# Performance work log

Hardware: AMD Instinct MI355X
Metric: run time of the kernel (lower is better)

The kernel has to match this reference:

```python
import jax, jax.numpy as jnp
import numpy as np

TEMPERATURE = 1.0
W_BLEND = 0.8
EPS = 1e-12  # torch F.normalize eps


def _l2norm(x):
    n = jnp.sqrt(jnp.sum(x * x, axis=-1, keepdims=True))
    return x / jnp.maximum(n, EPS)


def setup_inputs() -> dict:
    key = jax.random.key(0)
    feats = jax.random.normal(key, (4, 2048, 256), dtype=jnp.float32)
    return {"feats": feats}


def reference(feats):
    B, N, C = feats.shape
    f = _l2norm(feats.reshape(B * N, C))                 # [BN, C], unit rows
    scores = jnp.matmul(f, f.T) / TEMPERATURE            # [BN, BN] cosine sims
    attn = jax.nn.softmax(scores, axis=-1)               # [BN, BN]
    feats_att = jnp.matmul(attn, f)                      # [BN, C]
    feats_fcm = f * W_BLEND + feats_att * (1.0 - W_BLEND)
    return _l2norm(feats_fcm.reshape(B, N, C))           # [B, N, C]
```

## Files before the change

kernel.cpp:

```cpp
#include <hip/hip_runtime.h>

typedef unsigned char u8;
typedef unsigned short u16;
typedef unsigned int u32;
typedef unsigned long long u64;
typedef long long i64;
typedef __attribute__((ext_vector_type(16))) float floatx16;

#define BN 8192
#define DIM 256
#define NSPLIT 8
#define KPS (BN / NSPLIT)
#define BKN 32
#define NIT (KPS / BKN)

__device__ __forceinline__ u16 f2bf(float x) {
    u32 u = __builtin_bit_cast(u32, x);
    u = (u + 0x7fffu + ((u >> 16) & 1u)) >> 16;
    return (u16)u;
}
__device__ __forceinline__ float bf2f(u16 h) {
    return __builtin_bit_cast(float, (u32)h << 16);
}
__device__ __forceinline__ u64 pack4bf(float a, float b, float c, float d) {
    return (u64)f2bf(a) | ((u64)f2bf(b) << 16) | ((u64)f2bf(c) << 32) | ((u64)f2bf(d) << 48);
}
__device__ __forceinline__ u32 pk_fp8(float a, float b, float c, float d) {
    int v = __builtin_amdgcn_cvt_pk_fp8_f32(a, b, 0, false);
    v = __builtin_amdgcn_cvt_pk_fp8_f32(c, d, v, true);
    return (u32)v;
}
__device__ __forceinline__ void gl_lds16(const void* g, void* l) {
    __builtin_amdgcn_global_load_lds(
        (const __attribute__((address_space(1))) u32*)g,
        (__attribute__((address_space(3))) u32*)l, 16, 0, 0);
}
#define MFMA8(A, B, C) __builtin_amdgcn_mfma_f32_32x32x16_fp8_fp8((A), (B), (C), 0, 0, 0)

__global__ __launch_bounds__(256) void k_prep(const float* __restrict__ in,
                                              u8* __restrict__ fb, u8* __restrict__ fv) {
    __shared__ u16 t[32 * 260];
    const int tid = threadIdx.x;
    const int wave = tid >> 6, lane = tid & 63;
    const int kb = blockIdx.x, r0 = kb * 32;
    #pragma unroll
    for (int i = 0; i < 8; ++i) {
        const int rl = wave * 8 + i;
        const float4 v = *(const float4*)(in + (size_t)(r0 + rl) * DIM + lane * 4);
        float ss = v.x * v.x + v.y * v.y + v.z * v.z + v.w * v.w;
        #pragma unroll
        for (int off = 1; off < 64; off <<= 1) ss += __shfl_xor(ss, off, 64);
        const float inv = 1.0f / fmaxf(sqrtf(ss), 1e-12f);
        const float n0 = v.x * inv, n1 = v.y * inv, n2 = v.z * inv, n3 = v.w * inv;
        *(u32*)(fb + (size_t)(r0 + rl) * DIM + lane * 4) = pk_fp8(n0, n1, n2, n3);
        *(u64*)(&t[rl * 260 + lane * 4]) = pack4bf(n0, n1, n2, n3);
    }
    __syncthreads();
    #pragma unroll
    for (int i = 0; i < 4; ++i) {
        const int S = i * 256 + tid;
        const int d = S >> 2;
        const int c = ((S & 3) - (d >> 2)) & 3;
        float f[8];
        #pragma unroll
        for (int j = 0; j < 8; ++j) f[j] = bf2f(t[(8 * c + j) * 260 + d]);
        const u32 lo = pk_fp8(f[0], f[1], f[2], f[3]);
        const u32 hi = pk_fp8(f[4], f[5], f[6], f[7]);
        *(u64*)(fv + (size_t)kb * 8192 + S * 8) = ((u64)hi << 32) | lo;
    }
}

__global__ __launch_bounds__(256, 2) void k_flash(
        const u8* __restrict__ fb, const u8* __restrict__ fv,
        u16* __restrict__ Opart, float* __restrict__ lpart) {
    __shared__ u8 tileK[2][8192];
    __shared__ u8 tileV[2][8192];

    const int tid = threadIdx.x;
    const int wave = tid >> 6, lane = tid & 63;
    const int c31 = lane & 31, g1 = lane >> 5;
    const int split = blockIdx.x & (NSPLIT - 1);
    const int qblk = blockIdx.x >> 3;
    const int q0 = qblk * 128 + wave * 32;
    const int key0 = split * KPS;

    i64 qf[16];
    #pragma unroll
    for (int kc = 0; kc < 16; ++kc)
        qf[kc] = *(const i64*)(fb + (size_t)(q0 + c31) * DIM + kc * 16 + g1 * 8);

    floatx16 o[8];
    #pragma unroll
    for (int i = 0; i < 8; ++i)
        #pragma unroll
        for (int r = 0; r < 16; ++r) o[i][r] = 0.f;
    float lsum = 0.f;

    int offK[2];
    #pragma unroll
    for (int i = 0; i < 2; ++i) {
        const int S = wave * 128 + i * 64 + lane;
        const int r = S >> 4, s = S & 15;
        const int c = (s & 8) | ((s ^ r) & 7);
        offK[i] = r * 256 + c * 16;
    }
    const u8* gK = fb + (size_t)key0 * DIM;
    const u8* gV = fv + (size_t)(key0 >> 5) * 8192;

    auto stage = [&](int s, int b) {
        const size_t oo = (size_t)s * 8192;
        u8* lK = &tileK[b][0] + wave * 2048;
        u8* lV = &tileV[b][0] + wave * 2048;
        #pragma unroll
        for (int i = 0; i < 2; ++i) gl_lds16(gK + oo + offK[i], lK + i * 1024);
        #pragma unroll
        for (int i = 0; i < 2; ++i)
            gl_lds16(gV + oo + wave * 2048 + i * 1024 + lane * 16, lV + i * 1024);
    };

    const int cswA = (g1 + (c31 >> 2)) & 3;
    const int cswB = (2 + g1 + (c31 >> 2)) & 3;
    const int kx = (c31 & 7) << 4;

    stage(0, 0);
    for (int it = 0; it < NIT; ++it) {
        const int b = it & 1;
        __syncthreads();
        if (it + 1 < NIT) stage(it + 1, b ^ 1);

        const u8* tk = &tileK[b][0];
        const u8* tv = &tileV[b][0];
        const u8* bk = tk + c31 * 256 + g1 * 8;

        floatx16 s;
        #pragma unroll
        for (int r = 0; r < 16; ++r) s[r] = 0.f;

        i64 kf[8], vfa[8];
        #pragma unroll
        for (int j = 0; j < 8; ++j)
            kf[j] = *(const i64*)(bk + (kx ^ (j << 4)));
        #pragma unroll
        for (int dp = 0; dp < 4; ++dp) {
            const u8* ba = tv + (((dp * 2) * 32 + c31) * 4 + cswA) * 8;
            vfa[2 * dp] = *(const i64*)(ba);
            vfa[2 * dp + 1] = *(const i64*)(ba + 1024);
        }
        #pragma unroll
        for (int j = 0; j < 8; ++j) s = MFMA8(kf[j], qf[j], s);

        i64 vfb[8];
        #pragma unroll
        for (int j = 0; j < 8; ++j)
            kf[j] = *(const i64*)(bk + 128 + (kx ^ (j << 4)));
        #pragma unroll
        for (int dp = 0; dp < 4; ++dp) {
            const u8* ba = tv + (((dp * 2) * 32 + c31) * 4 + cswB) * 8;
            vfb[2 * dp] = *(const i64*)(ba);
            vfb[2 * dp + 1] = *(const i64*)(ba + 1024);
        }
        #pragma unroll
        for (int j = 0; j < 8; ++j) s = MFMA8(kf[j], qf[8 + j], s);

        const float e0 = __expf(s[0]), e1 = __expf(s[1]), e2 = __expf(s[2]), e3 = __expf(s[3]);
        const float e4 = __expf(s[4]), e5 = __expf(s[5]), e6 = __expf(s[6]), e7 = __expf(s[7]);
        const u32 p0 = pk_fp8(e0, e1, e2, e3);
        const u32 p1 = pk_fp8(e4, e5, e6, e7);
        const u32 x0 = (u32)__shfl_xor((int)(g1 ? p0 : p1), 32, 64);
        const i64 A0 = g1 ? (i64)(((u64)p1 << 32) | x0) : (i64)(((u64)x0 << 32) | p0);

        o[0] = MFMA8(A0, vfa[0], o[0]);
        const float e8 = __expf(s[8]), e9 = __expf(s[9]);
        o[1] = MFMA8(A0, vfa[1], o[1]);
        const float e10 = __expf(s[10]), e11 = __expf(s[11]);
        o[2] = MFMA8(A0, vfa[2], o[2]);
        const float e12 = __expf(s[12]), e13 = __expf(s[13]);
        o[3] = MFMA8(A0, vfa[3], o[3]);
        const float e14 = __expf(s[14]), e15 = __expf(s[15]);
        o[4] = MFMA8(A0, vfa[4], o[4]);
        const u32 p2 = pk_fp8(e8, e9, e10, e11);
        lsum += (e0 + e1) + (e2 + e3);
        o[5] = MFMA8(A0, vfa[5], o[5]);
        const u32 p3 = pk_fp8(e12, e13, e14, e15);
        lsum += (e4 + e5) + (e6 + e7);
        o[6] = MFMA8(A0, vfa[6], o[6]);
        const u32 x1 = (u32)__shfl_xor((int)(g1 ? p2 : p3), 32, 64);
        lsum += (e8 + e9) + (e10 + e11);
        o[7] = MFMA8(A0, vfa[7], o[7]);
        const i64 A1 = g1 ? (i64)(((u64)p3 << 32) | x1) : (i64)(((u64)x1 << 32) | p2);
        lsum += (e12 + e13) + (e14 + e15);

        #pragma unroll
        for (int ds = 0; ds < 8; ++ds) o[ds] = MFMA8(A1, vfb[ds], o[ds]);
    }

    u16* ob = Opart + ((size_t)split * BN + q0) * DIM;
    #pragma unroll
    for (int ds = 0; ds < 8; ++ds) {
        #pragma unroll
        for (int r = 0; r < 16; ++r) {
            const int ql = (r & 3) + 8 * (r >> 2) + 4 * g1;
            ob[(size_t)ql * DIM + ds * 32 + c31] = f2bf(o[ds][r]);
        }
    }
    lsum += __shfl_xor(lsum, 32, 64);
    if (g1 == 0) lpart[(size_t)split * BN + q0 + c31] = lsum;
}

__global__ __launch_bounds__(256) void k_combine(
        const float* __restrict__ feats, const u16* __restrict__ Opart,
        const float* __restrict__ lpart, float* __restrict__ out) {
    const int row = blockIdx.x * 4 + (threadIdx.x >> 6);
    const int lane = threadIdx.x & 63;

    float L = 0.f;
    #pragma unroll
    for (int s = 0; s < NSPLIT; ++s) L += lpart[(size_t)s * BN + row];

    float a0 = 0.f, a1 = 0.f, a2 = 0.f, a3 = 0.f;
    #pragma unroll
    for (int s = 0; s < NSPLIT; ++s) {
        const ushort4 o = *(const ushort4*)(Opart + ((size_t)s * BN + row) * DIM + lane * 4);
        a0 += bf2f(o.x); a1 += bf2f(o.y); a2 += bf2f(o.z); a3 += bf2f(o.w);
    }
    const float invL = 1.0f / L;

    const float4 v = *(const float4*)(feats + (size_t)row * DIM + lane * 4);
    float ss = v.x * v.x + v.y * v.y + v.z * v.z + v.w * v.w;
    #pragma unroll
    for (int off = 1; off < 64; off <<= 1) ss += __shfl_xor(ss, off, 64);
    const float invf = 1.0f / fmaxf(sqrtf(ss), 1e-12f);

    const float yx = 0.8f * v.x * invf + 0.2f * a0 * invL;
    const float yy = 0.8f * v.y * invf + 0.2f * a1 * invL;
    const float yz = 0.8f * v.z * invf + 0.2f * a2 * invL;
    const float yw = 0.8f * v.w * invf + 0.2f * a3 * invL;

    float s2 = yx * yx + yy * yy + yz * yz + yw * yw;
    #pragma unroll
    for (int off = 1; off < 64; off <<= 1) s2 += __shfl_xor(s2, off, 64);
    const float invn = 1.0f / fmaxf(sqrtf(s2), 1e-12f);

    float4 o; o.x = yx * invn; o.y = yy * invn; o.z = yz * invn; o.w = yw * invn;
    *(float4*)(out + (size_t)row * DIM + lane * 4) = o;
}

extern "C" void kernel_launch(void* const* d_in, const int* in_sizes, int n_in,
                              void* d_out, int out_size, void* d_ws, size_t ws_size,
                              hipStream_t stream) {
    const float* feats = (const float*)d_in[0];
    float* out = (float*)d_out;
    char* ws = (char*)d_ws;

    u8* fb = (u8*)ws;
    u8* fv = (u8*)(ws + (size_t)BN * DIM);
    u16* Op = (u16*)(ws + (size_t)BN * DIM * 2);
    float* lp = (float*)(ws + (size_t)BN * DIM * 2 + (size_t)NSPLIT * BN * DIM * 2);

    k_prep<<<BN / 32, 256, 0, stream>>>(feats, fb, fv);
    k_flash<<<(BN / 128) * NSPLIT, 256, 0, stream>>>(fb, fv, Op, lp);
    k_combine<<<BN / 4, 256, 0, stream>>>(feats, Op, lp, out);
}
```

Baseline: 130.9 us.

## Double key tile per iteration, prefetch next subtile K, add MFMA priority hints

Each main-loop iteration of the flash kernel now processes 64 keys instead of 32 by handling two 32-key subtiles, which halves the number of __syncthreads barriers and stage calls. K fragments for the second subtile are read from LDS while the first subtile's last PV MFMAs run, and s_setprio hints raise wave priority around the MFMA runs. In exchange, LDS per block doubles to 64 KB, which may limit occupancy under the 2-blocks-per-CU launch bound, and register pressure rises from the extra kf2 array.

```diff
diff --git a/kernel.cpp b/kernel.cpp
--- a/kernel.cpp
+++ b/kernel.cpp
@@ -11,7 +11,7 @@
 #define DIM 256
 #define NSPLIT 8
 #define KPS (BN / NSPLIT)
-#define BKN 32
+#define BKN 64
 #define NIT (KPS / BKN)
 
 __device__ __forceinline__ u16 f2bf(float x) {
@@ -73,8 +73,8 @@
 __global__ __launch_bounds__(256, 2) void k_flash(
         const u8* __restrict__ fb, const u8* __restrict__ fv,
         u16* __restrict__ Opart, float* __restrict__ lpart) {
-    __shared__ u8 tileK[2][8192];
-    __shared__ u8 tileV[2][8192];
+    __shared__ u8 tileK[2][16384];
+    __shared__ u8 tileV[2][16384];
 
     const int tid = threadIdx.x;
     const int wave = tid >> 6, lane = tid & 63;
@@ -96,10 +96,10 @@
         for (int r = 0; r < 16; ++r) o[i][r] = 0.f;
     float lsum = 0.f;
 
-    int offK[2];
-    #pragma unroll
-    for (int i = 0; i < 2; ++i) {
-        const int S = wave * 128 + i * 64 + lane;
+    int offK[4];
+    #pragma unroll
+    for (int i = 0; i < 4; ++i) {
+        const int S = wave * 256 + i * 64 + lane;
         const int r = S >> 4, s = S & 15;
         const int c = (s & 8) | ((s ^ r) & 7);
         offK[i] = r * 256 + c * 16;
@@ -108,14 +108,15 @@
     const u8* gV = fv + (size_t)(key0 >> 5) * 8192;
 
     auto stage = [&](int s, int b) {
-        const size_t oo = (size_t)s * 8192;
-        u8* lK = &tileK[b][0] + wave * 2048;
-        u8* lV = &tileV[b][0] + wave * 2048;
-        #pragma unroll
-        for (int i = 0; i < 2; ++i) gl_lds16(gK + oo + offK[i], lK + i * 1024);
-        #pragma unroll
-        for (int i = 0; i < 2; ++i)
-            gl_lds16(gV + oo + wave * 2048 + i * 1024 + lane * 16, lV + i * 1024);
+        const size_t oo = (size_t)s * 16384;
+        u8* lK = &tileK[b][0];
+        u8* lV = &tileV[b][0] + wave * 4096;
+        #pragma unroll
+        for (int i = 0; i < 4; ++i)
+            gl_lds16(gK + oo + offK[i], lK + wave * 4096 + i * 1024);
+        #pragma unroll
+        for (int i = 0; i < 4; ++i)
+            gl_lds16(gV + oo + wave * 4096 + i * 1024 + lane * 16, lV + i * 1024);
     };
 
     const int cswA = (g1 + (c31 >> 2)) & 3;
@@ -123,6 +124,7 @@
     const int kx = (c31 & 7) << 4;
 
     stage(0, 0);
+    i64 kf2[8];
     for (int it = 0; it < NIT; ++it) {
         const int b = it & 1;
         __syncthreads();
@@ -130,68 +132,148 @@
 
         const u8* tk = &tileK[b][0];
         const u8* tv = &tileV[b][0];
-        const u8* bk = tk + c31 * 256 + g1 * 8;
-
-        floatx16 s;
-        #pragma unroll
-        for (int r = 0; r < 16; ++r) s[r] = 0.f;
-
-        i64 kf[8], vfa[8];
-        #pragma unroll
-        for (int j = 0; j < 8; ++j)
-            kf[j] = *(const i64*)(bk + (kx ^ (j << 4)));
-        #pragma unroll
-        for (int dp = 0; dp < 4; ++dp) {
-            const u8* ba = tv + (((dp * 2) * 32 + c31) * 4 + cswA) * 8;
-            vfa[2 * dp] = *(const i64*)(ba);
-            vfa[2 * dp + 1] = *(const i64*)(ba + 1024);
+        const u8* bk0 = tk + c31 * 256 + g1 * 8;
+        const u8* bk1 = tk + 8192 + c31 * 256 + g1 * 8;
+        const u8* tv1 = tv + 8192;
+
+        {
+            floatx16 s;
+            #pragma unroll
+            for (int r = 0; r < 16; ++r) s[r] = 0.f;
+
+            i64 kf[8], vfa[8], vfb[8];
+            #pragma unroll
+            for (int j = 0; j < 8; ++j)
+                kf[j] = *(const i64*)(bk0 + (kx ^ (j << 4)));
+            #pragma unroll
+            for (int dp = 0; dp < 4; ++dp) {
+                const u8* ba = tv + (((dp * 2) * 32 + c31) * 4 + cswA) * 8;
+                vfa[2 * dp] = *(const i64*)(ba);
+                vfa[2 * dp + 1] = *(const i64*)(ba + 1024);
+            }
+            __builtin_amdgcn_s_setprio(1);
+            #pragma unroll
+            for (int j = 0; j < 8; ++j) s = MFMA8(kf[j], qf[j], s);
+            __builtin_amdgcn_s_setprio(0);
+
+            #pragma unroll
+            for (int j = 0; j < 8; ++j)
+                kf[j] = *(const i64*)(bk0 + 128 + (kx ^ (j << 4)));
+            #pragma unroll
+            for (int dp = 0; dp < 4; ++dp) {
+                const u8* ba = tv + (((dp * 2) * 32 + c31) * 4 + cswB) * 8;
+                vfb[2 * dp] = *(const i64*)(ba);
+                vfb[2 * dp + 1] = *(const i64*)(ba + 1024);
+            }
+            __builtin_amdgcn_s_setprio(1);
+            #pragma unroll
+            for (int j = 0; j < 8; ++j) s = MFMA8(kf[j], qf[8 + j], s);
+            __builtin_amdgcn_s_setprio(0);
+
+            const float e0 = __expf(s[0]), e1 = __expf(s[1]), e2 = __expf(s[2]), e3 = __expf(s[3]);
+            const float e4 = __expf(s[4]), e5 = __expf(s[5]), e6 = __expf(s[6]), e7 = __expf(s[7]);
+            const u32 p0 = pk_fp8(e0, e1, e2, e3);
+            const u32 p1 = pk_fp8(e4, e5, e6, e7);
+            const u32 x0 = (u32)__shfl_xor((int)(g1 ? p0 : p1), 32, 64);
+            const i64 A0 = g1 ? (i64)(((u64)p1 << 32) | x0) : (i64)(((u64)x0 << 32) | p0);
+
+            o[0] = MFMA8(A0, vfa[0], o[0]);
+            const float e8 = __expf(s[8]), e9 = __expf(s[9]);
+            o[1] = MFMA8(A0, vfa[1], o[1]);
+            const float e10 = __expf(s[10]), e11 = __expf(s[11]);
+            o[2] = MFMA8(A0, vfa[2], o[2]);
+            const float e12 = __expf(s[12]), e13 = __expf(s[13]);
+            o[3] = MFMA8(A0, vfa[3], o[3]);
+            const float e14 = __expf(s[14]), e15 = __expf(s[15]);
+            o[4] = MFMA8(A0, vfa[4], o[4]);
+            const u32 p2 = pk_fp8(e8, e9, e10, e11);
+            lsum += (e0 + e1) + (e2 + e3);
+            o[5] = MFMA8(A0, vfa[5], o[5]);
+            const u32 p3 = pk_fp8(e12, e13, e14, e15);
+            lsum += (e4 + e5) + (e6 + e7);
+            o[6] = MFMA8(A0, vfa[6], o[6]);
+            const u32 x1 = (u32)__shfl_xor((int)(g1 ? p2 : p3), 32, 64);
+            lsum += (e8 + e9) + (e10 + e11);
+            o[7] = MFMA8(A0, vfa[7], o[7]);
+            const i64 A1 = g1 ? (i64)(((u64)p3 << 32) | x1) : (i64)(((u64)x1 << 32) | p2);
+            lsum += (e12 + e13) + (e14 + e15);
+
+            __builtin_amdgcn_s_setprio(1);
+            o[0] = MFMA8(A1, vfb[0], o[0]); kf2[0] = *(const i64*)(bk1 + (kx ^ 0));
+            o[1] = MFMA8(A1, vfb[1], o[1]); kf2[1] = *(const i64*)(bk1 + (kx ^ 16));
+            o[2] = MFMA8(A1, vfb[2], o[2]); kf2[2] = *(const i64*)(bk1 + (kx ^ 32));
+            o[3] = MFMA8(A1, vfb[3], o[3]); kf2[3] = *(const i64*)(bk1 + (kx ^ 48));
+            o[4] = MFMA8(A1, vfb[4], o[4]); kf2[4] = *(const i64*)(bk1 + (kx ^ 64));
+            o[5] = MFMA8(A1, vfb[5], o[5]); kf2[5] = *(const i64*)(bk1 + (kx ^ 80));
+            o[6] = MFMA8(A1, vfb[6], o[6]); kf2[6] = *(const i64*)(bk1 + (kx ^ 96));
+            o[7] = MFMA8(A1, vfb[7], o[7]); kf2[7] = *(const i64*)(bk1 + (kx ^ 112));
+            __builtin_amdgcn_s_setprio(0);
         }
-        #pragma unroll
-        for (int j = 0; j < 8; ++j) s = MFMA8(kf[j], qf[j], s);
-
-        i64 vfb[8];
-        #pragma unroll
-        for (int j = 0; j < 8; ++j)
-            kf[j] = *(const i64*)(bk + 128 + (kx ^ (j << 4)));
-        #pragma unroll
-        for (int dp = 0; dp < 4; ++dp) {
-            const u8* ba = tv + (((dp * 2) * 32 + c31) * 4 + cswB) * 8;
-            vfb[2 * dp] = *(const i64*)(ba);
-            vfb[2 * dp + 1] = *(const i64*)(ba + 1024);
+
+        {
+            floatx16 s;
+            #pragma unroll
+            for (int r = 0; r < 16; ++r) s[r] = 0.f;
+
+            i64 kf[8], vfa[8], vfb[8];
+            #pragma unroll
+            for (int dp = 0; dp < 4; ++dp) {
+                const u8* ba = tv1 + (((dp * 2) * 32 + c31) * 4 + cswA) * 8;
+                vfa[2 * dp] = *(const i64*)(ba);
+                vfa[2 * dp + 1] = *(const i64*)(ba + 1024);
+            }
+            __builtin_amdgcn_s_setprio(1);
+            #pragma unroll
+            for (int j = 0; j < 8; ++j) s = MFMA8(kf2[j], qf[j], s);
+            __builtin_amdgcn_s_setprio(0);
+
+            #pragma unroll
+            for (int j = 0; j < 8; ++j)
+                kf[j] = *(const i64*)(bk1 + 128 + (kx ^ (j << 4)));
+            #pragma unroll
+            for (int dp = 0; dp < 4; ++dp) {
+                const u8* ba = tv1 + (((dp * 2) * 32 + c31) * 4 + cswB) * 8;
+                vfb[2 * dp] = *(const i64*)(ba);
+                vfb[2 * dp + 1] = *(const i64*)(ba + 1024);
+            }
+            __builtin_amdgcn_s_setprio(1);
+            #pragma unroll
+            for (int j = 0; j < 8; ++j) s = MFMA8(kf[j], qf[8 + j], s);
+            __builtin_amdgcn_s_setprio(0);
+
+            const float e0 = __expf(s[0]), e1 = __expf(s[1]), e2 = __expf(s[2]), e3 = __expf(s[3]);
+            const float e4 = __expf(s[4]), e5 = __expf(s[5]), e6 = __expf(s[6]), e7 = __expf(s[7]);
+            const u32 p0 = pk_fp8(e0, e1, e2, e3);
+            const u32 p1 = pk_fp8(e4, e5, e6, e7);
+            const u32 x0 = (u32)__shfl_xor((int)(g1 ? p0 : p1), 32, 64);
+            const i64 A0 = g1 ? (i64)(((u64)p1 << 32) | x0) : (i64)(((u64)x0 << 32) | p0);
+
+            o[0] = MFMA8(A0, vfa[0], o[0]);
+            const float e8 = __expf(s[8]), e9 = __expf(s[9]);
+            o[1] = MFMA8(A0, vfa[1], o[1]);
+            const float e10 = __expf(s[10]), e11 = __expf(s[11]);
+            o[2] = MFMA8(A0, vfa[2], o[2]);
+            const float e12 = __expf(s[12]), e13 = __expf(s[13]);
+            o[3] = MFMA8(A0, vfa[3], o[3]);
+            const float e14 = __expf(s[14]), e15 = __expf(s[15]);
+            o[4] = MFMA8(A0, vfa[4], o[4]);
+            const u32 p2 = pk_fp8(e8, e9, e10, e11);
+            lsum += (e0 + e1) + (e2 + e3);
+            o[5] = MFMA8(A0, vfa[5], o[5]);
+            const u32 p3 = pk_fp8(e12, e13, e14, e15);
+            lsum += (e4 + e5) + (e6 + e7);
+            o[6] = MFMA8(A0, vfa[6], o[6]);
+            const u32 x1 = (u32)__shfl_xor((int)(g1 ? p2 : p3), 32, 64);
+            lsum += (e8 + e9) + (e10 + e11);
+            o[7] = MFMA8(A0, vfa[7], o[7]);
+            const i64 A1 = g1 ? (i64)(((u64)p3 << 32) | x1) : (i64)(((u64)x1 << 32) | p2);
+            lsum += (e12 + e13) + (e14 + e15);
+
+            __builtin_amdgcn_s_setprio(1);
+            #pragma unroll
+            for (int ds = 0; ds < 8; ++ds) o[ds] = MFMA8(A1, vfb[ds], o[ds]);
+            __builtin_amdgcn_s_setprio(0);
         }
-        #pragma unroll
-        for (int j = 0; j < 8; ++j) s = MFMA8(kf[j], qf[8 + j], s);
-
-        const float e0 = __expf(s[0]), e1 = __expf(s[1]), e2 = __expf(s[2]), e3 = __expf(s[3]);
-        const float e4 = __expf(s[4]), e5 = __expf(s[5]), e6 = __expf(s[6]), e7 = __expf(s[7]);
-        const u32 p0 = pk_fp8(e0, e1, e2, e3);
-        const u32 p1 = pk_fp8(e4, e5, e6, e7);
-        const u32 x0 = (u32)__shfl_xor((int)(g1 ? p0 : p1), 32, 64);
-        const i64 A0 = g1 ? (i64)(((u64)p1 << 32) | x0) : (i64)(((u64)x0 << 32) | p0);
-
-        o[0] = MFMA8(A0, vfa[0], o[0]);
-        const float e8 = __expf(s[8]), e9 = __expf(s[9]);
-        o[1] = MFMA8(A0, vfa[1], o[1]);
-        const float e10 = __expf(s[10]), e11 = __expf(s[11]);
-        o[2] = MFMA8(A0, vfa[2], o[2]);
-        const float e12 = __expf(s[12]), e13 = __expf(s[13]);
-        o[3] = MFMA8(A0, vfa[3], o[3]);
-        const float e14 = __expf(s[14]), e15 = __expf(s[15]);
-        o[4] = MFMA8(A0, vfa[4], o[4]);
-        const u32 p2 = pk_fp8(e8, e9, e10, e11);
-        lsum += (e0 + e1) + (e2 + e3);
-        o[5] = MFMA8(A0, vfa[5], o[5]);
-        const u32 p3 = pk_fp8(e12, e13, e14, e15);
-        lsum += (e4 + e5) + (e6 + e7);
-        o[6] = MFMA8(A0, vfa[6], o[6]);
-        const u32 x1 = (u32)__shfl_xor((int)(g1 ? p2 : p3), 32, 64);
-        lsum += (e8 + e9) + (e10 + e11);
-        o[7] = MFMA8(A0, vfa[7], o[7]);
-        const i64 A1 = g1 ? (i64)(((u64)p3 << 32) | x1) : (i64)(((u64)x1 << 32) | p2);
-        lsum += (e12 + e13) + (e14 + e15);
-
-        #pragma unroll
-        for (int ds = 0; ds < 8; ++ds) o[ds] = MFMA8(A1, vfb[ds], o[ds]);
     }
 
     u16* ob = Opart + ((size_t)split * BN + q0) * DIM;
```

New measurement: 138.5 us. +5.8%, slower.

## Fuse split-K combine into flash kernel via last-block atomic ticket

Applied to the files above, without the earlier changes.

Removes the separate combine kernel. Each flash block bumps a per-query-block atomic ticket after writing its partial output, and the last of the split blocks for that query block reduces all partials and applies the blend and normalization. This saves a kernel launch and lets the combine overlap with other flash blocks, but adds a memset launch, threadfences, and a serial 32-row tail handled by only 64 blocks.

```diff
diff --git a/kernel.cpp b/kernel.cpp
--- a/kernel.cpp
+++ b/kernel.cpp
@@ -13,6 +13,7 @@
 #define KPS (BN / NSPLIT)
 #define BKN 32
 #define NIT (KPS / BKN)
+#define NQB (BN / 128)
 
 __device__ __forceinline__ u16 f2bf(float x) {
     u32 u = __builtin_bit_cast(u32, x);
@@ -72,9 +73,12 @@
 
 __global__ __launch_bounds__(256, 2) void k_flash(
         const u8* __restrict__ fb, const u8* __restrict__ fv,
-        u16* __restrict__ Opart, float* __restrict__ lpart) {
+        const float* __restrict__ feats,
+        u16* __restrict__ Opart, float* __restrict__ lpart,
+        u32* __restrict__ ticket, float* __restrict__ out) {
     __shared__ u8 tileK[2][8192];
     __shared__ u8 tileV[2][8192];
+    __shared__ int s_last;
 
     const int tid = threadIdx.x;
     const int wave = tid >> 6, lane = tid & 63;
@@ -205,44 +209,51 @@
     }
     lsum += __shfl_xor(lsum, 32, 64);
     if (g1 == 0) lpart[(size_t)split * BN + q0 + c31] = lsum;
-}
-
-__global__ __launch_bounds__(256) void k_combine(
-        const float* __restrict__ feats, const u16* __restrict__ Opart,
-        const float* __restrict__ lpart, float* __restrict__ out) {
-    const int row = blockIdx.x * 4 + (threadIdx.x >> 6);
-    const int lane = threadIdx.x & 63;
-
-    float L = 0.f;
-    #pragma unroll
-    for (int s = 0; s < NSPLIT; ++s) L += lpart[(size_t)s * BN + row];
-
-    float a0 = 0.f, a1 = 0.f, a2 = 0.f, a3 = 0.f;
-    #pragma unroll
-    for (int s = 0; s < NSPLIT; ++s) {
-        const ushort4 o = *(const ushort4*)(Opart + ((size_t)s * BN + row) * DIM + lane * 4);
-        a0 += bf2f(o.x); a1 += bf2f(o.y); a2 += bf2f(o.z); a3 += bf2f(o.w);
-    }
-    const float invL = 1.0f / L;
-
-    const float4 v = *(const float4*)(feats + (size_t)row * DIM + lane * 4);
-    float ss = v.x * v.x + v.y * v.y + v.z * v.z + v.w * v.w;
-    #pragma unroll
-    for (int off = 1; off < 64; off <<= 1) ss += __shfl_xor(ss, off, 64);
-    const float invf = 1.0f / fmaxf(sqrtf(ss), 1e-12f);
-
-    const float yx = 0.8f * v.x * invf + 0.2f * a0 * invL;
-    const float yy = 0.8f * v.y * invf + 0.2f * a1 * invL;
-    const float yz = 0.8f * v.z * invf + 0.2f * a2 * invL;
-    const float yw = 0.8f * v.w * invf + 0.2f * a3 * invL;
-
-    float s2 = yx * yx + yy * yy + yz * yz + yw * yw;
-    #pragma unroll
-    for (int off = 1; off < 64; off <<= 1) s2 += __shfl_xor(s2, off, 64);
-    const float invn = 1.0f / fmaxf(sqrtf(s2), 1e-12f);
-
-    float4 o; o.x = yx * invn; o.y = yy * invn; o.z = yz * invn; o.w = yw * invn;
-    *(float4*)(out + (size_t)row * DIM + lane * 4) = o;
+
+    __threadfence();
+    __syncthreads();
+    if (tid == 0) s_last = (atomicAdd(&ticket[qblk], 1u) == NSPLIT - 1);
+    __syncthreads();
+    if (s_last) {
+        __threadfence();
+        const int rowbase = qblk * 128;
+        #pragma unroll 1
+        for (int rr = 0; rr < 32; ++rr) {
+            const int row = rowbase + wave * 32 + rr;
+
+            float L = 0.f;
+            #pragma unroll
+            for (int s = 0; s < NSPLIT; ++s) L += lpart[(size_t)s * BN + row];
+
+            float a0 = 0.f, a1 = 0.f, a2 = 0.f, a3 = 0.f;
+            #pragma unroll
+            for (int s = 0; s < NSPLIT; ++s) {
+                const ushort4 ov = *(const ushort4*)(Opart + ((size_t)s * BN + row) * DIM + lane * 4);
+                a0 += bf2f(ov.x); a1 += bf2f(ov.y); a2 += bf2f(ov.z); a3 += bf2f(ov.w);
+            }
+            const float invL = 1.0f / L;
+
+            const float4 v = *(const float4*)(feats + (size_t)row * DIM + lane * 4);
+            float ss = v.x * v.x + v.y * v.y + v.z * v.z + v.w * v.w;
+            #pragma unroll
+            for (int off = 1; off < 64; off <<= 1) ss += __shfl_xor(ss, off, 64);
+            const float invf = 1.0f / fmaxf(sqrtf(ss), 1e-12f);
+
+            const float yx = 0.8f * v.x * invf + 0.2f * a0 * invL;
+            const float yy = 0.8f * v.y * invf + 0.2f * a1 * invL;
+            const float yz = 0.8f * v.z * invf + 0.2f * a2 * invL;
+            const float yw = 0.8f * v.w * invf + 0.2f * a3 * invL;
+
+            float s2 = yx * yx + yy * yy + yz * yz + yw * yw;
+            #pragma unroll
+            for (int off = 1; off < 64; off <<= 1) s2 += __shfl_xor(s2, off, 64);
+            const float invn = 1.0f / fmaxf(sqrtf(s2), 1e-12f);
+
+            float4 ovec; ovec.x = yx * invn; ovec.y = yy * invn;
+            ovec.z = yz * invn; ovec.w = yw * invn;
+            *(float4*)(out + (size_t)row * DIM + lane * 4) = ovec;
+        }
+    }
 }
 
 extern "C" void kernel_launch(void* const* d_in, const int* in_sizes, int n_in,
@@ -256,8 +267,10 @@
     u8* fv = (u8*)(ws + (size_t)BN * DIM);
     u16* Op = (u16*)(ws + (size_t)BN * DIM * 2);
     float* lp = (float*)(ws + (size_t)BN * DIM * 2 + (size_t)NSPLIT * BN * DIM * 2);
-
+    u32* tk = (u32*)(ws + (size_t)BN * DIM * 2 + (size_t)NSPLIT * BN * DIM * 2
+                        + (size_t)NSPLIT * BN * 4);
+
+    hipMemsetAsync(tk, 0, NQB * sizeof(u32), stream);
     k_prep<<<BN / 32, 256, 0, stream>>>(feats, fb, fv);
-    k_flash<<<(BN / 128) * NSPLIT, 256, 0, stream>>>(fb, fv, Op, lp);
-    k_combine<<<BN / 4, 256, 0, stream>>>(feats, Op, lp, out);
-}
+    k_flash<<<NQB * NSPLIT, 256, 0, stream>>>(fb, fv, feats, Op, lp, tk, out);
+}
```

Result: slower. 253.3 us (+93.5%).
